# Performance work log

Hardware: AMD Instinct MI355X
Metric: run time of the kernel (lower is better)

The kernel has to match this reference:

```python
import jax, jax.numpy as jnp
import numpy as np
from jax import lax

B, L, D_MODEL = 2, 1024, 1024
EXPAND, D_STATE, D_CONV = 2, 16, 4
D_INNER = EXPAND * D_MODEL
DT_RANK = D_MODEL // 16  # ceil(1024/16) = 64
D_FF = 4 * D_MODEL


def setup_inputs() -> dict:
    key = jax.random.key(0)
    ks = jax.random.split(key, 20)
    s = lambda *sh: 1.0 / np.sqrt(sh[-1])
    inp = {
        "x": jax.random.normal(ks[0], (B, L, D_MODEL), jnp.float32),
        "ln1_w": jnp.ones((D_MODEL,), jnp.float32),
        "ln1_b": jnp.zeros((D_MODEL,), jnp.float32),
        "W_in": jax.random.normal(ks[1], (2 * D_INNER, D_MODEL), jnp.float32) * s(D_MODEL),
        "conv_w": jax.random.normal(ks[2], (D_INNER, D_CONV), jnp.float32) * s(D_CONV),
        "conv_b": jnp.zeros((D_INNER,), jnp.float32),
        "W_xproj": jax.random.normal(ks[3], (DT_RANK + 2 * D_STATE, D_INNER), jnp.float32) * s(D_INNER),
        "W_dt": jax.random.normal(ks[4], (D_INNER, DT_RANK), jnp.float32) * s(DT_RANK),
        "b_dt": jax.random.uniform(ks[5], (D_INNER,), jnp.float32, -4.0, -2.0),  # dt bias ~ small softplus
        "A_log": jnp.log(jnp.broadcast_to(jnp.arange(1, D_STATE + 1, dtype=jnp.float32), (D_INNER, D_STATE))),
        "D": jnp.ones((D_INNER,), jnp.float32),
        "W_out": jax.random.normal(ks[6], (D_MODEL, D_INNER), jnp.float32) * s(D_INNER),
        "ln2_w": jnp.ones((D_MODEL,), jnp.float32),
        "ln2_b": jnp.zeros((D_MODEL,), jnp.float32),
        "W1": jax.random.normal(ks[7], (D_FF, D_MODEL), jnp.float32) * s(D_MODEL),
        "b1": jnp.zeros((D_FF,), jnp.float32),
        "W2": jax.random.normal(ks[8], (D_MODEL, D_FF), jnp.float32) * s(D_FF),
        "b2": jnp.zeros((D_MODEL,), jnp.float32),
    }
    return inp


def _layernorm(x, w, b, eps=1e-5):
    mu = jnp.mean(x, axis=-1, keepdims=True)
    var = jnp.var(x, axis=-1, keepdims=True)
    return (x - mu) * lax.rsqrt(var + eps) * w + b


def _mamba(h, W_in, conv_w, conv_b, W_xproj, W_dt, b_dt, A_log, D, W_out):
    # in_proj -> [B, L, 2*d_inner]
    xz = jnp.einsum("bld,ed->ble", h, W_in)
    u, z = xz[..., :D_INNER], xz[..., D_INNER:]
    # causal depthwise conv over time
    uc = jnp.transpose(u, (0, 2, 1))  # [B, d_inner, L]
    uc = lax.conv_general_dilated(
        uc, conv_w[:, None, :], window_strides=(1,), padding=[(D_CONV - 1, 0)],
        dimension_numbers=("NCH", "OIH", "NCH"), feature_group_count=D_INNER)
    uc = jax.nn.silu(uc + conv_b[None, :, None])
    u = jnp.transpose(uc, (0, 2, 1))  # [B, L, d_inner]
    # input-dependent dt, B, C
    x_db = jnp.einsum("bld,ed->ble", u, W_xproj)
    dt = jax.nn.softplus(jnp.einsum("blr,dr->bld", x_db[..., :DT_RANK], W_dt) + b_dt)
    Bm = x_db[..., DT_RANK:DT_RANK + D_STATE]  # [B, L, d_state]
    Cm = x_db[..., DT_RANK + D_STATE:]         # [B, L, d_state]
    A = -jnp.exp(A_log)                        # [d_inner, d_state]

    def step(hst, t):
        dt_t, B_t, C_t, u_t = t  # [B,d_inner], [B,ds], [B,ds], [B,d_inner]
        dA = jnp.exp(dt_t[:, :, None] * A)                       # [B,d_inner,d_state]
        hst = dA * hst + dt_t[:, :, None] * B_t[:, None, :] * u_t[:, :, None]
        y_t = jnp.einsum("bds,bs->bd", hst, C_t)
        return hst, y_t

    h0 = jnp.zeros((u.shape[0], D_INNER, D_STATE), u.dtype)
    xs = (jnp.swapaxes(dt, 0, 1), jnp.swapaxes(Bm, 0, 1), jnp.swapaxes(Cm, 0, 1), jnp.swapaxes(u, 0, 1))
    _, ys = lax.scan(step, h0, xs)
    y = jnp.swapaxes(ys, 0, 1) + u * D  # skip term D*u
    y = y * jax.nn.silu(z)
    return jnp.einsum("ble,de->bld", y, W_out)


def reference(x, ln1_w, ln1_b, W_in, conv_w, conv_b, W_xproj, W_dt, b_dt, A_log, D,
              W_out, ln2_w, ln2_b, W1, b1, W2, b2):
    x = x + _mamba(_layernorm(x, ln1_w, ln1_b), W_in, conv_w, conv_b, W_xproj, W_dt, b_dt, A_log, D, W_out)
    h = _layernorm(x, ln2_w, ln2_b)
    ffn = jnp.einsum("blf,df->bld", jax.nn.relu(jnp.einsum("bld,fd->blf", h, W1) + b1), W2) + b2
    return x + ffn
```

## Files before the change

kernel.cpp:

```cpp
#include <hip/hip_runtime.h>

typedef unsigned short u16;
typedef unsigned int   u32;
typedef short   bf16x8 __attribute__((ext_vector_type(8)));
typedef float   f32x4  __attribute__((ext_vector_type(4)));
typedef u16     u16x4  __attribute__((ext_vector_type(4)));

__device__ __forceinline__ u16 f2b(float f) {
    u32 u = __builtin_bit_cast(u32, f);
    u32 r = u + 0x7FFFu + ((u >> 16) & 1u);
    return (u16)(r >> 16);
}
__device__ __forceinline__ float b2f(u16 h) {
    u32 u = ((u32)h) << 16;
    return __builtin_bit_cast(float, u);
}
__device__ __forceinline__ u16x4 f4_to_b4(float4 v) {
    u16x4 o; o.x = f2b(v.x); o.y = f2b(v.y); o.z = f2b(v.z); o.w = f2b(v.w);
    return o;
}

__device__ __forceinline__ float fexp2(float x) {
    float r;
    asm("v_exp_f32 %0, %1" : "=v"(r) : "v"(x));
    return r;
}
__device__ __forceinline__ float flog2(float x) {
    float r;
    asm("v_log_f32 %0, %1" : "=v"(r) : "v"(x));
    return r;
}

template <int CTRL>
__device__ __forceinline__ float dpp_add(float p) {
    int pi = __builtin_bit_cast(int, p);
    int q  = __builtin_amdgcn_update_dpp(pi, pi, CTRL, 0xF, 0xF, false);
    return p + __builtin_bit_cast(float, q);
}
#define DPP_XOR1 0xB1
#define DPP_XOR2 0x4E
#define DPP_HMIR 0x141
#define DPP_MIR  0x140

#define MROWS   2048
#define NSEG    16
#define SEGT    64
#define L2E     1.44269504088896340736f
#define LN2     0.69314718055994530942f

#define GLDS(g, l) __builtin_amdgcn_global_load_lds(                      \
    (const __attribute__((address_space(1))) void*)(g),                   \
    (__attribute__((address_space(3))) void*)(l), 16, 0, 0)

__global__ __launch_bounds__(256) void cvt_kernel(const float* __restrict__ in,
                                                  u16* __restrict__ out, int n4) {
    int i = blockIdx.x * 256 + threadIdx.x;
    if (i < n4) {
        float4 v = ((const float4*)in)[i];
        ((u16x4*)out)[i] = f4_to_b4(v);
    }
}

__global__ __launch_bounds__(256) void pad_xproj_kernel(const float* __restrict__ in,
                                                        u16* __restrict__ out) {
    int i = blockIdx.x * 256 + threadIdx.x;
    int r = i >> 9, c4 = i & 511;
    float4 v = make_float4(0.f, 0.f, 0.f, 0.f);
    if (r < 96) v = ((const float4*)(in + (size_t)r * 2048))[c4];
    ((u16x4*)(out + (size_t)r * 2048))[c4] = f4_to_b4(v);
}

__global__ __launch_bounds__(256) void ln_kernel(const float* __restrict__ x,
                                                 const float* __restrict__ w,
                                                 const float* __restrict__ b,
                                                 u16* __restrict__ out) {
    const int row = blockIdx.x;
    const int tid = threadIdx.x;
    const float4 v = ((const float4*)(x + (size_t)row * 1024))[tid];
    float s = v.x + v.y + v.z + v.w;
    float q = v.x * v.x + v.y * v.y + v.z * v.z + v.w * v.w;
#pragma unroll
    for (int off = 1; off < 64; off <<= 1) {
        s += __shfl_xor(s, off, 64);
        q += __shfl_xor(q, off, 64);
    }
    __shared__ float ss[4], qq[4];
    const int wave = tid >> 6;
    if ((tid & 63) == 0) { ss[wave] = s; qq[wave] = q; }
    __syncthreads();
    s = ss[0] + ss[1] + ss[2] + ss[3];
    q = qq[0] + qq[1] + qq[2] + qq[3];
    const float mean = s * (1.f / 1024.f);
    const float var  = q * (1.f / 1024.f) - mean * mean;
    const float rstd = rsqrtf(var + 1e-5f);
    const float4 wv = ((const float4*)w)[tid];
    const float4 bv = ((const float4*)b)[tid];
    float4 o;
    o.x = (v.x - mean) * rstd * wv.x + bv.x;
    o.y = (v.y - mean) * rstd * wv.y + bv.y;
    o.z = (v.z - mean) * rstd * wv.z + bv.z;
    o.w = (v.w - mean) * rstd * wv.w + bv.w;
    ((u16x4*)(out + (size_t)row * 1024))[tid] = f4_to_b4(o);
}

__global__ __launch_bounds__(256) void conv_kernel(const u16* __restrict__ xzu,
                                                   const float* __restrict__ cw,
                                                   const float* __restrict__ cb,
                                                   u16* __restrict__ up,
                                                   u16* __restrict__ utl) {
    const int idx = blockIdx.x * 256 + threadIdx.x;
    const int row = idx >> 9;
    const int d4  = idx & 511;
    const int d   = d4 * 4;
    const int bb  = row >> 10;
    const int t   = row & 1023;
    float w0[4], w1[4], w2[4], w3[4];
    *(float4*)w0 = ((const float4*)cw)[d + 0];
    *(float4*)w1 = ((const float4*)cw)[d + 1];
    *(float4*)w2 = ((const float4*)cw)[d + 2];
    *(float4*)w3 = ((const float4*)cw)[d + 3];
    float4 a = ((const float4*)cb)[d4];
#pragma unroll
    for (int j = 0; j < 4; ++j) {
        const int tt = t - 3 + j;
        if (tt >= 0) {
            const u16x4 uv = *(const u16x4*)(xzu + ((size_t)(bb * 1024 + tt)) * 2048 + d);
            a.x += b2f(uv.x) * w0[j];
            a.y += b2f(uv.y) * w1[j];
            a.z += b2f(uv.z) * w2[j];
            a.w += b2f(uv.w) * w3[j];
        }
    }
    float4 o;
    o.x = a.x / (1.f + __expf(-a.x));
    o.y = a.y / (1.f + __expf(-a.y));
    o.z = a.z / (1.f + __expf(-a.z));
    o.w = a.w / (1.f + __expf(-a.w));
    const u16x4 pk = f4_to_b4(o);
    ((u16x4*)up)[idx] = pk;
    *(u16x4*)(utl + (((size_t)(d >> 4)) * 2048 + row) * 16 + (d & 15)) = pk;
}

__global__ __launch_bounds__(256) void gemm_tb(const u16* __restrict__ A,
                                               const u16* __restrict__ Bw,
                                               float* __restrict__ Cptr,
                                               int M, int N, int K, int KS) {
    const int nbm = gridDim.x, nbn = gridDim.y;
    const int nwg = nbm * nbn;
    const int id  = blockIdx.x + nbm * blockIdx.y;
    const int sw  = (nwg >= 8) ? ((id & 7) * (nwg >> 3) + (id >> 3)) : id;
    const int bm  = sw % nbm, bn = sw / nbm;

    __shared__ u16 Asm[3][128 * 32];
    __shared__ u16 Bsm[3][128 * 32];
    const int tid  = threadIdx.x;
    const int kz   = blockIdx.z;
    const int lane = tid & 63;
    const int wave = tid >> 6;
    const int wm   = wave >> 1, wn = wave & 1;
    const u16* Ag = A  + (size_t)bm * 128 * K;
    const u16* Bg = Bw + (size_t)bn * 128 * K;
    const int r0 = tid >> 2;
    const int r1 = r0 + 64;
    const int sg = (tid & 3) * 8;
    const int k0 = kz * KS;
    const int nk = KS >> 5;
    const int fr = lane & 15, fk = (lane >> 4) * 8;

#define STG(bf, kk)                                                            \
    {                                                                          \
        const int kof = k0 + (kk) * 32;                                        \
        GLDS(Ag + (size_t)r0 * K + kof + sg, &Asm[bf][tid * 8]);               \
        GLDS(Ag + (size_t)r1 * K + kof + sg, &Asm[bf][(tid + 256) * 8]);       \
        GLDS(Bg + (size_t)r0 * K + kof + sg, &Bsm[bf][tid * 8]);               \
        GLDS(Bg + (size_t)r1 * K + kof + sg, &Bsm[bf][(tid + 256) * 8]);       \
    }

    f32x4 acc[4][4] = {};
    STG(0, 0); STG(1, 1); STG(2, 2);
    int buf = 0;
    for (int k = 0; k < nk; ++k) {
        if (k < nk - 2)       asm volatile("s_waitcnt vmcnt(8)" ::: "memory");
        else if (k == nk - 2) asm volatile("s_waitcnt vmcnt(4)" ::: "memory");
        else                  asm volatile("s_waitcnt vmcnt(0)" ::: "memory");
        __builtin_amdgcn_s_barrier();
        bf16x8 a[4], b[4];
#pragma unroll
        for (int m = 0; m < 4; ++m)
            a[m] = *(const bf16x8*)&Asm[buf][(wm * 64 + m * 16 + fr) * 32 + fk];
#pragma unroll
        for (int n = 0; n < 4; ++n)
            b[n] = *(const bf16x8*)&Bsm[buf][(wn * 64 + n * 16 + fr) * 32 + fk];
        asm volatile("s_waitcnt lgkmcnt(0)" ::: "memory");
        __builtin_amdgcn_s_barrier();
        if (k + 3 < nk) STG(buf, k + 3);
#pragma unroll
        for (int m = 0; m < 4; ++m)
#pragma unroll
            for (int n = 0; n < 4; ++n)
                acc[m][n] = __builtin_amdgcn_mfma_f32_16x16x32_bf16(a[m], b[n], acc[m][n], 0, 0, 0);
        buf = (buf == 2) ? 0 : buf + 1;
    }
#undef STG

    const int fq = lane >> 4;
#pragma unroll
    for (int m = 0; m < 4; ++m) {
#pragma unroll
        for (int n = 0; n < 4; ++n) {
            const int row0 = bm * 128 + wm * 64 + m * 16 + fq * 4;
            const int col  = bn * 128 + wn * 64 + n * 16 + fr;
#pragma unroll
            for (int j = 0; j < 4; ++j)
                Cptr[(size_t)kz * M * N + (size_t)(row0 + j) * N + col] = acc[m][n][j];
        }
    }
}

template <int EPI>
__global__ __launch_bounds__(256) void gemm_a64(const u16* __restrict__ A,
                                                const u16* __restrict__ Bw,
                                                void* __restrict__ Cptr,
                                                void* __restrict__ Cptr2,
                                                const float* __restrict__ bias,
                                                int M, int N, int K) {
    const int nbm = gridDim.x, nbn = gridDim.y;
    const int nwg = nbm * nbn;
    const int id  = blockIdx.x + nbm * blockIdx.y;
    const int sw  = (id & 7) * (nwg >> 3) + (id >> 3);
    const int bm  = sw % nbm, bn = sw / nbm;

    __shared__ u16 Asm[3][64 * 32];
    __shared__ u16 Bsm[3][128 * 32];
    const int tid  = threadIdx.x;
    const int lane = tid & 63;
    const int wave = tid >> 6;
    const int wm   = wave >> 1, wn = wave & 1;
    const u16* Ag = A  + (size_t)bm * 64 * K;
    const u16* Bg = Bw + (size_t)bn * 128 * K;
    const int r0 = tid >> 2;
    const int r1 = r0 + 64;
    const int sg = (tid & 3) * 8;
    const int nk = K >> 5;
    const int fr = lane & 15, fk = (lane >> 4) * 8;

#define STGA(bf, kk)                                                           \
    {                                                                          \
        const int kof = (kk) * 32;                                             \
        GLDS(Ag + (size_t)r0 * K + kof + sg, &Asm[bf][tid * 8]);               \
        GLDS(Bg + (size_t)r0 * K + kof + sg, &Bsm[bf][tid * 8]);               \
        GLDS(Bg + (size_t)r1 * K + kof + sg, &Bsm[bf][(tid + 256) * 8]);       \
    }

    f32x4 acc[2][4] = {};
    STGA(0, 0); STGA(1, 1); STGA(2, 2);
    int buf = 0;
    for (int k = 0; k < nk; ++k) {
        if (k < nk - 2)       asm volatile("s_waitcnt vmcnt(6)" ::: "memory");
        else if (k == nk - 2) asm volatile("s_waitcnt vmcnt(3)" ::: "memory");
        else                  asm volatile("s_waitcnt vmcnt(0)" ::: "memory");
        __builtin_amdgcn_s_barrier();
        bf16x8 a[2], b[4];
#pragma unroll
        for (int m = 0; m < 2; ++m)
            a[m] = *(const bf16x8*)&Asm[buf][(wm * 32 + m * 16 + fr) * 32 + fk];
#pragma unroll
        for (int n = 0; n < 4; ++n)
            b[n] = *(const bf16x8*)&Bsm[buf][(wn * 64 + n * 16 + fr) * 32 + fk];
        asm volatile("s_waitcnt lgkmcnt(0)" ::: "memory");
        __builtin_amdgcn_s_barrier();
        if (k + 3 < nk) STGA(buf, k + 3);
#pragma unroll
        for (int m = 0; m < 2; ++m)
#pragma unroll
            for (int n = 0; n < 4; ++n)
                acc[m][n] = __builtin_amdgcn_mfma_f32_16x16x32_bf16(a[m], b[n], acc[m][n], 0, 0, 0);
        buf = (buf == 2) ? 0 : buf + 1;
    }
#undef STGA

    const int fq = lane >> 4;
#pragma unroll
    for (int m = 0; m < 2; ++m) {
#pragma unroll
        for (int n = 0; n < 4; ++n) {
            const int row0 = bm * 64 + wm * 32 + m * 16 + fq * 4;
            const int col  = bn * 128 + wn * 64 + n * 16 + fr;
#pragma unroll
            for (int j = 0; j < 4; ++j) {
                float v = acc[m][n][j];
                if constexpr (EPI == 3) {
                    v += bias[col];
                    ((u16*)Cptr)[(size_t)(row0 + j) * N + col] = f2b(fmaxf(v, 0.f));
                } else {
                    if (col < 2048) {
                        ((u16*)Cptr)[(size_t)(row0 + j) * 2048 + col] = f2b(v);
                    } else {
                        const float sv = v / (1.f + __expf(-v));
                        const int zc = col - 2048;
                        ((u16*)Cptr2)[(((size_t)(zc >> 4)) * 2048 + row0 + j) * 16 + (zc & 15)]
                            = f2b(sv);
                    }
                }
            }
        }
    }
}

__global__ __launch_bounds__(256) void xproj_combine(const float* __restrict__ part,
                                                     u16* __restrict__ xdbr,
                                                     float* __restrict__ bcp) {
    int i = blockIdx.x * 256 + threadIdx.x;
    int row = i >> 5, c4 = i & 31;
    if (c4 >= 24) return;
    float4 s = make_float4(0.f, 0.f, 0.f, 0.f);
#pragma unroll
    for (int p = 0; p < 8; ++p) {
        float4 v = ((const float4*)(part + (size_t)p * MROWS * 128 + (size_t)row * 128))[c4];
        s.x += v.x; s.y += v.y; s.z += v.z; s.w += v.w;
    }
    if (c4 < 16) {
        ((u16x4*)(xdbr + (size_t)row * 64))[c4] = f4_to_b4(s);
    } else {
        const int e0 = (c4 - 16) * 4;
        float sv[4] = {s.x, s.y, s.z, s.w};
#pragma unroll
        for (int j = 0; j < 4; ++j) {
            const int e = e0 + j;
            const int st  = (e < 16) ? e : (e - 16);
            const int isc = (e < 16) ? 0 : 1;
            bcp[(size_t)(row >> 1) * 64 + st * 4 + (row & 1) * 2 + isc] = sv[j];
        }
    }
}

__device__ __forceinline__ void compute_dtu_tile(const u16* __restrict__ xdbr,
                                                 const u16* __restrict__ Wdtb,
                                                 const float* __restrict__ b_dt,
                                                 const u16* __restrict__ utile,
                                                 float* __restrict__ du_s,
                                                 size_t t0, int d0, int w, int l) {
    const int fr = l & 15, fk = (l >> 4) * 8;
    const bf16x8 a0 = *(const bf16x8*)(xdbr + (t0 + w * 16 + fr) * 64 + fk);
    const bf16x8 a1 = *(const bf16x8*)(xdbr + (t0 + w * 16 + fr) * 64 + 32 + fk);
    const bf16x8 b0 = *(const bf16x8*)(Wdtb + (size_t)(d0 + fr) * 64 + fk);
    const bf16x8 b1 = *(const bf16x8*)(Wdtb + (size_t)(d0 + fr) * 64 + 32 + fk);
    const float bdt = b_dt[d0 + fr];
    f32x4 acc = {};
    acc = __builtin_amdgcn_mfma_f32_16x16x32_bf16(a0, b0, acc, 0, 0, 0);
    acc = __builtin_amdgcn_mfma_f32_16x16x32_bf16(a1, b1, acc, 0, 0, 0);
#pragma unroll
    for (int j = 0; j < 4; ++j) {
        const int row = w * 16 + (l >> 4) * 4 + j;
        float v = acc[j] + bdt;
        const float sp = flog2(1.f + fexp2(v * L2E)) * LN2;
        v = (v > 20.f) ? v : sp;
        const float uval = b2f(utile[(t0 + row) * 16 + fr]);
        float2 dv; dv.x = v; dv.y = v * uval;
        *(float2*)&du_s[(row >> 1) * 66 + fr * 4 + (row & 1) * 2] = dv;
    }
}

__device__ __forceinline__ void stage_bc(const float* __restrict__ bcp,
                                         float* __restrict__ bc_s,
                                         size_t p0, int w, int l) {
    const int pr = (w << 3) + (l >> 4);
    const int pc = (l & 15) << 2;
    GLDS(bcp + (p0 + pr) * 64 + pc,     &bc_s[(w << 9)]);
    GLDS(bcp + (p0 + pr + 4) * 64 + pc, &bc_s[(w << 9) + 256]);
}

__global__ __launch_bounds__(256) void scan_pass1(const u16* __restrict__ xdbr,
                                                  const u16* __restrict__ Wdtb,
                                                  const float* __restrict__ b_dt,
                                                  const u16* __restrict__ utl,
                                                  const float* __restrict__ bcp,
                                                  const float* __restrict__ A_log,
                                                  float* __restrict__ Qarr,
                                                  float* __restrict__ Sarr) {
    __shared__ __align__(16) float du_s[32 * 66];
    __shared__ __align__(16) float bc_s[32 * 64];

    const int tid = threadIdx.x;
    const int l   = tid & 63;
    const int w   = tid >> 6;
    const int s   = l & 15;
    const int g   = (w << 2) | (l >> 4);
    const int d0  = blockIdx.x << 4;
    const int b   = blockIdx.y;
    const int seg = blockIdx.z;
    const int d   = d0 + g;
    const size_t t0 = (size_t)b * 1024 + (size_t)seg * SEGT;
    const u16* utile = utl + (size_t)(d0 >> 4) * 2048 * 16;

    stage_bc(bcp, bc_s, t0 >> 1, w, l);
    compute_dtu_tile(xdbr, Wdtb, b_dt, utile, du_s, t0, d0, w, l);

    const float As2 = -__expf(A_log[d * 16 + s]) * L2E;
    asm volatile("s_waitcnt vmcnt(0) lgkmcnt(0)" ::: "memory");
    __builtin_amdgcn_s_barrier();

    float Q = 0.f, S = 0.f;
#pragma unroll 8
    for (int t2 = 0; t2 < 32; ++t2) {
        const float4 du4 = *(const float4*)&du_s[t2 * 66 + g * 4];
        const float4 BC2 = *(const float4*)&bc_s[t2 * 64 + s * 4];
        S += du4.x;
        Q = fexp2(du4.x * As2) * Q + du4.y * BC2.x;
        S += du4.z;
        Q = fexp2(du4.z * As2) * Q + du4.w * BC2.z;
    }
    Qarr[(((size_t)seg * 2 + b) * 2048 + d) * 16 + s] = Q;
    if (s == 0) Sarr[((size_t)seg * 2 + b) * 2048 + d] = S;
}

__global__ __launch_bounds__(256) void scan_prefix(const float* __restrict__ Qarr,
                                                   const float* __restrict__ Sarr,
                                                   const float* __restrict__ A_log,
                                                   float* __restrict__ H0) {
    const int tid = threadIdx.x;
    const int d   = (blockIdx.x << 4) + (tid >> 4);
    const int s   = tid & 15;
    const int b   = blockIdx.y;
    const float As2 = -__expf(A_log[d * 16 + s]) * L2E;
    float h = 0.f;
#pragma unroll
    for (int i = 0; i < NSEG; ++i) {
        const size_t base = ((size_t)i * 2 + b) * 2048 + d;
        H0[base * 16 + s] = h;
        h = fexp2(As2 * Sarr[base]) * h + Qarr[base * 16 + s];
    }
}

__global__ __launch_bounds__(256) void scan_pass2(const u16* __restrict__ xdbr,
                                                  const u16* __restrict__ Wdtb,
                                                  const float* __restrict__ b_dt,
                                                  const u16* __restrict__ utl,
                                                  const float* __restrict__ bcp,
                                                  const u16* __restrict__ zst,
                                                  const float* __restrict__ A_log,
                                                  const float* __restrict__ Dp,
                                                  const float* __restrict__ H0,
                                                  u16* __restrict__ ymul) {
    __shared__ __align__(16) float du_s[32 * 66];
    __shared__ __align__(16) float bc_s[32 * 64];
    __shared__ __align__(16) u16   u_s[1024];
    __shared__ __align__(16) u16   z_s[1024];

    const int tid = threadIdx.x;
    const int l   = tid & 63;
    const int w   = tid >> 6;
    const int s   = l & 15;
    const int g   = (w << 2) | (l >> 4);
    const int d0  = blockIdx.x << 4;
    const int b   = blockIdx.y;
    const int seg = blockIdx.z;
    const int d   = d0 + g;
    const size_t t0 = (size_t)b * 1024 + (size_t)seg * SEGT;
    const u16* utile = utl + (size_t)(d0 >> 4) * 2048 * 16;
    const u16* ztile = zst + (size_t)(d0 >> 4) * 2048 * 16;

    stage_bc(bcp, bc_s, t0 >> 1, w, l);
    if (w < 2)
        GLDS(utile + t0 * 16 + ((w & 1) * 64 + l) * 8, &u_s[(w & 1) << 9]);
    else
        GLDS(ztile + t0 * 16 + ((w & 1) * 64 + l) * 8, &z_s[(w & 1) << 9]);

    compute_dtu_tile(xdbr, Wdtb, b_dt, utile, du_s, t0, d0, w, l);

    const float As2 = -__expf(A_log[d * 16 + s]) * L2E;
    float h = H0[(((size_t)seg * 2 + b) * 2048 + d) * 16 + s];

    asm volatile("s_waitcnt vmcnt(0) lgkmcnt(0)" ::: "memory");
    __builtin_amdgcn_s_barrier();

    float pk[4];
#pragma unroll
    for (int c = 0; c < 4; ++c) {
        pk[c] = 0.f;
#pragma unroll
        for (int q = 0; q < 8; ++q) {
            const int t2 = c * 8 + q;
            const float4 du4 = *(const float4*)&du_s[t2 * 66 + g * 4];
            const float4 BC2 = *(const float4*)&bc_s[t2 * 64 + s * 4];
            h = fexp2(du4.x * As2) * h + du4.y * BC2.x;
            float p = h * BC2.y;
            p = dpp_add<DPP_XOR1>(p);
            p = dpp_add<DPP_XOR2>(p);
            p = dpp_add<DPP_HMIR>(p);
            p = dpp_add<DPP_MIR>(p);
            {
                const unsigned long long km = 0x0001000100010001ULL << (2 * q);
                asm("v_cndmask_b32 %0, %0, %1, %2" : "+v"(pk[c]) : "v"(p), "s"(km));
            }
            h = fexp2(du4.z * As2) * h + du4.w * BC2.z;
            p = h * BC2.w;
            p = dpp_add<DPP_XOR1>(p);
            p = dpp_add<DPP_XOR2>(p);
            p = dpp_add<DPP_HMIR>(p);
            p = dpp_add<DPP_MIR>(p);
            {
                const unsigned long long km = 0x0001000100010001ULL << (2 * q + 1);
                asm("v_cndmask_b32 %0, %0, %1, %2" : "+v"(pk[c]) : "v"(p), "s"(km));
            }
        }
    }

    __builtin_amdgcn_s_barrier();
    float* p_s = du_s;
#pragma unroll
    for (int c = 0; c < 4; ++c) {
        const int row = c * 16 + s;
        p_s[row * 16 + (g ^ (row & 12))] = pk[c];
    }

    asm volatile("s_waitcnt lgkmcnt(0)" ::: "memory");
    __builtin_amdgcn_s_barrier();

    {
        const int tt = tid >> 2, cc = (tid & 3) << 2;
        const float4 pv = *(const float4*)&p_s[tt * 16 + (cc ^ (tt & 12))];
        const u16x4  uv = *(const u16x4*)&u_s[tt * 16 + cc];
        const u16x4  zs = *(const u16x4*)&z_s[tt * 16 + cc];
        const float4 Dv = *(const float4*)(Dp + d0 + cc);
        float4 o;
        o.x = (pv.x + b2f(uv.x) * Dv.x) * b2f(zs.x);
        o.y = (pv.y + b2f(uv.y) * Dv.y) * b2f(zs.y);
        o.z = (pv.z + b2f(uv.z) * Dv.z) * b2f(zs.z);
        o.w = (pv.w + b2f(uv.w) * Dv.w) * b2f(zs.w);
        *(u16x4*)(ymul + (t0 + tt) * 2048 + d0 + cc) = f4_to_b4(o);
    }
}

__global__ __launch_bounds__(256) void ffn2_combine(const float* __restrict__ part,
                                                    const float* __restrict__ x2,
                                                    const float* __restrict__ b2,
                                                    float* __restrict__ out) {
    int i = blockIdx.x * 256 + threadIdx.x;
    float4 s = ((const float4*)x2)[i];
    float4 bv = ((const float4*)b2)[i & 255];
    s.x += bv.x; s.y += bv.y; s.z += bv.z; s.w += bv.w;
#pragma unroll
    for (int p = 0; p < 4; ++p) {
        float4 v = ((const float4*)(part + (size_t)p * MROWS * 1024))[i];
        s.x += v.x; s.y += v.y; s.z += v.z; s.w += v.w;
    }
    ((float4*)out)[i] = s;
}

__global__ __launch_bounds__(256) void outproj_combine_ln2(const float* __restrict__ x,
                                                           const float* __restrict__ part,
                                                           const float* __restrict__ w,
                                                           const float* __restrict__ b,
                                                           float* __restrict__ x2,
                                                           u16* __restrict__ h2) {
    const int row = blockIdx.x;
    const int tid = threadIdx.x;
    float4 v = ((const float4*)(x + (size_t)row * 1024))[tid];
    float4 p0 = ((const float4*)(part + (size_t)row * 1024))[tid];
    float4 p1 = ((const float4*)(part + (size_t)MROWS * 1024 + (size_t)row * 1024))[tid];
    v.x += p0.x + p1.x; v.y += p0.y + p1.y; v.z += p0.z + p1.z; v.w += p0.w + p1.w;
    ((float4*)(x2 + (size_t)row * 1024))[tid] = v;
    float s = v.x + v.y + v.z + v.w;
    float q = v.x * v.x + v.y * v.y + v.z * v.z + v.w * v.w;
#pragma unroll
    for (int off = 1; off < 64; off <<= 1) {
        s += __shfl_xor(s, off, 64);
        q += __shfl_xor(q, off, 64);
    }
    __shared__ float ss[4], qq[4];
    const int wave = tid >> 6;
    if ((tid & 63) == 0) { ss[wave] = s; qq[wave] = q; }
    __syncthreads();
    s = ss[0] + ss[1] + ss[2] + ss[3];
    q = qq[0] + qq[1] + qq[2] + qq[3];
    const float mean = s * (1.f / 1024.f);
    const float var  = q * (1.f / 1024.f) - mean * mean;
    const float rstd = rsqrtf(var + 1e-5f);
    const float4 wv = ((const float4*)w)[tid];
    const float4 bv = ((const float4*)b)[tid];
    float4 o;
    o.x = (v.x - mean) * rstd * wv.x + bv.x;
    o.y = (v.y - mean) * rstd * wv.y + bv.y;
    o.z = (v.z - mean) * rstd * wv.z + bv.z;
    o.w = (v.w - mean) * rstd * wv.w + bv.w;
    ((u16x4*)(h2 + (size_t)row * 1024))[tid] = f4_to_b4(o);
}

extern "C" void kernel_launch(void* const* d_in, const int* in_sizes, int n_in,
                              void* d_out, int out_size, void* d_ws, size_t ws_size,
                              hipStream_t stream) {
    const float* x      = (const float*)d_in[0];
    const float* ln1_w  = (const float*)d_in[1];
    const float* ln1_b  = (const float*)d_in[2];
    const float* W_in   = (const float*)d_in[3];
    const float* conv_w = (const float*)d_in[4];
    const float* conv_b = (const float*)d_in[5];
    const float* W_xproj= (const float*)d_in[6];
    const float* W_dt   = (const float*)d_in[7];
    const float* b_dt   = (const float*)d_in[8];
    const float* A_log  = (const float*)d_in[9];
    const float* Dvec   = (const float*)d_in[10];
    const float* W_out  = (const float*)d_in[11];
    const float* ln2_w  = (const float*)d_in[12];
    const float* ln2_b  = (const float*)d_in[13];
    const float* W1     = (const float*)d_in[14];
    const float* b1     = (const float*)d_in[15];
    const float* W2     = (const float*)d_in[16];
    const float* b2     = (const float*)d_in[17];
    float* out = (float*)d_out;
    char*  ws  = (char*)d_ws;
    const size_t MB = 1024ull * 1024ull;

    u16*   h1b   = (u16*)(ws + 0);
    u16*   xzu   = (u16*)(ws + 4 * MB);
    u16*   zst   = (u16*)(ws + 12 * MB);
    u16*   upb   = (u16*)(ws + 20 * MB);
    u16*   utl   = (u16*)(ws + 28 * MB);
    float* parts = (float*)(ws + 36 * MB);
    float* bcp   = (float*)(ws + 44 * MB);
    u16*   xdbr  = (u16*)(ws + 44 * MB + 256 * 1024);
    u16*   Wdtb  = (u16*)(ws + 44 * MB + 512 * 1024);
    u16*   ymul  = (u16*)(ws + 45 * MB);
    float* Qarr  = (float*)(ws + 53 * MB);
    float* Sarr  = (float*)(ws + 57 * MB);
    float* H0    = (float*)(ws + 58 * MB);
    float* x2    = (float*)(ws + 62 * MB);
    u16*   Winb  = (u16*)(ws + 70 * MB);
    u16*   Woutb = (u16*)(ws + 78 * MB);
    u16*   W1b   = (u16*)(ws + 82 * MB);
    u16*   W2b   = (u16*)(ws + 90 * MB);
    u16*   Wxpb  = (u16*)(ws + 98 * MB);
    u16*   h2b   = h1b;
    float* opart = (float*)(ws + 4 * MB);
    u16*   f1    = (u16*)(ws + 4 * MB);
    float* fpart = (float*)(ws + 20 * MB);

    cvt_kernel<<<4096, 256, 0, stream>>>(W_in,  Winb,  4096 * 1024 / 4);
    cvt_kernel<<<2048, 256, 0, stream>>>(W_out, Woutb, 1024 * 2048 / 4);
    cvt_kernel<<<4096, 256, 0, stream>>>(W1,    W1b,   4096 * 1024 / 4);
    cvt_kernel<<<4096, 256, 0, stream>>>(W2,    W2b,   1024 * 4096 / 4);
    cvt_kernel<<<128,  256, 0, stream>>>(W_dt,  Wdtb,  2048 * 64 / 4);
    pad_xproj_kernel<<<256, 256, 0, stream>>>(W_xproj, Wxpb);

    ln_kernel<<<2048, 256, 0, stream>>>(x, ln1_w, ln1_b, h1b);
    gemm_a64<5><<<dim3(32, 32), 256, 0, stream>>>(h1b, Winb, xzu, zst, nullptr,
                                                  MROWS, 4096, 1024);
    conv_kernel<<<4096, 256, 0, stream>>>(xzu, conv_w, conv_b, upb, utl);
    gemm_tb<<<dim3(16, 1, 8), 256, 0, stream>>>(upb, Wxpb, parts, MROWS, 128, 2048, 256);
    xproj_combine<<<256, 256, 0, stream>>>(parts, xdbr, bcp);
    scan_pass1<<<dim3(128, 2, NSEG), 256, 0, stream>>>(xdbr, Wdtb, b_dt, utl, bcp, A_log,
                                                       Qarr, Sarr);
    scan_prefix<<<dim3(128, 2), 256, 0, stream>>>(Qarr, Sarr, A_log, H0);
    scan_pass2<<<dim3(128, 2, NSEG), 256, 0, stream>>>(xdbr, Wdtb, b_dt, utl, bcp, zst,
                                                       A_log, Dvec, H0, ymul);
    gemm_tb<<<dim3(16, 8, 2), 256, 0, stream>>>(ymul, Woutb, opart, MROWS, 1024, 2048, 1024);
    outproj_combine_ln2<<<2048, 256, 0, stream>>>(x, opart, ln2_w, ln2_b, x2, h2b);
    gemm_a64<3><<<dim3(32, 32), 256, 0, stream>>>(h2b, W1b, f1, nullptr, b1,
                                                  MROWS, 4096, 1024);
    gemm_tb<<<dim3(16, 8, 4), 256, 0, stream>>>(f1, W2b, fpart, MROWS, 1024, 4096, 1024);
    ffn2_combine<<<2048, 256, 0, stream>>>(fpart, x2, b2, out);
}
```

Baseline: 242.9 us.

## Unify GEMMs on 128x128 tiles, read x-proj from tiled conv output, merge weight casts

```diff
diff --git a/kernel.cpp b/kernel.cpp
--- a/kernel.cpp
+++ b/kernel.cpp
@@ -52,13 +52,25 @@
     (const __attribute__((address_space(1))) void*)(g),                   \
     (__attribute__((address_space(3))) void*)(l), 16, 0, 0)
 
-__global__ __launch_bounds__(256) void cvt_kernel(const float* __restrict__ in,
-                                                  u16* __restrict__ out, int n4) {
-    int i = blockIdx.x * 256 + threadIdx.x;
-    if (i < n4) {
-        float4 v = ((const float4*)in)[i];
-        ((u16x4*)out)[i] = f4_to_b4(v);
-    }
+__global__ __launch_bounds__(256) void cvt_all(const float* __restrict__ W_in,
+                                               const float* __restrict__ W_out,
+                                               const float* __restrict__ W1,
+                                               const float* __restrict__ W2,
+                                               const float* __restrict__ W_dt,
+                                               u16* __restrict__ Winb,
+                                               u16* __restrict__ Woutb,
+                                               u16* __restrict__ W1b,
+                                               u16* __restrict__ W2b,
+                                               u16* __restrict__ Wdtb) {
+    const int i = blockIdx.x * 256 + threadIdx.x;
+    const float* src; u16* dst; int off;
+    if (i < 1048576)      { src = W_in;  dst = Winb;  off = i; }
+    else if (i < 1572864) { src = W_out; dst = Woutb; off = i - 1048576; }
+    else if (i < 2621440) { src = W1;    dst = W1b;   off = i - 1572864; }
+    else if (i < 3670016) { src = W2;    dst = W2b;   off = i - 2621440; }
+    else                  { src = W_dt;  dst = Wdtb;  off = i - 3670016; }
+    float4 v = ((const float4*)src)[off];
+    ((u16x4*)dst)[off] = f4_to_b4(v);
 }
 
 __global__ __launch_bounds__(256) void pad_xproj_kernel(const float* __restrict__ in,
@@ -106,7 +118,6 @@
 __global__ __launch_bounds__(256) void conv_kernel(const u16* __restrict__ xzu,
                                                    const float* __restrict__ cw,
                                                    const float* __restrict__ cb,
-                                                   u16* __restrict__ up,
                                                    u16* __restrict__ utl) {
     const int idx = blockIdx.x * 256 + threadIdx.x;
     const int row = idx >> 9;
@@ -136,14 +147,15 @@
     o.y = a.y / (1.f + __expf(-a.y));
     o.z = a.z / (1.f + __expf(-a.z));
     o.w = a.w / (1.f + __expf(-a.w));
-    const u16x4 pk = f4_to_b4(o);
-    ((u16x4*)up)[idx] = pk;
-    *(u16x4*)(utl + (((size_t)(d >> 4)) * 2048 + row) * 16 + (d & 15)) = pk;
-}
-
+    *(u16x4*)(utl + (((size_t)(d >> 4)) * 2048 + row) * 16 + (d & 15)) = f4_to_b4(o);
+}
+
+template <int EPI>
 __global__ __launch_bounds__(256) void gemm_tb(const u16* __restrict__ A,
                                                const u16* __restrict__ Bw,
-                                               float* __restrict__ Cptr,
+                                               void* __restrict__ Cptr,
+                                               void* __restrict__ Cptr2,
+                                               const float* __restrict__ bias,
                                                int M, int N, int K, int KS) {
     const int nbm = gridDim.x, nbn = gridDim.y;
     const int nwg = nbm * nbn;
@@ -211,88 +223,12 @@
             const int row0 = bm * 128 + wm * 64 + m * 16 + fq * 4;
             const int col  = bn * 128 + wn * 64 + n * 16 + fr;
 #pragma unroll
-            for (int j = 0; j < 4; ++j)
-                Cptr[(size_t)kz * M * N + (size_t)(row0 + j) * N + col] = acc[m][n][j];
-        }
-    }
-}
-
-template <int EPI>
-__global__ __launch_bounds__(256) void gemm_a64(const u16* __restrict__ A,
-                                                const u16* __restrict__ Bw,
-                                                void* __restrict__ Cptr,
-                                                void* __restrict__ Cptr2,
-                                                const float* __restrict__ bias,
-                                                int M, int N, int K) {
-    const int nbm = gridDim.x, nbn = gridDim.y;
-    const int nwg = nbm * nbn;
-    const int id  = blockIdx.x + nbm * blockIdx.y;
-    const int sw  = (id & 7) * (nwg >> 3) + (id >> 3);
-    const int bm  = sw % nbm, bn = sw / nbm;
-
-    __shared__ u16 Asm[3][64 * 32];
-    __shared__ u16 Bsm[3][128 * 32];
-    const int tid  = threadIdx.x;
-    const int lane = tid & 63;
-    const int wave = tid >> 6;
-    const int wm   = wave >> 1, wn = wave & 1;
-    const u16* Ag = A  + (size_t)bm * 64 * K;
-    const u16* Bg = Bw + (size_t)bn * 128 * K;
-    const int r0 = tid >> 2;
-    const int r1 = r0 + 64;
-    const int sg = (tid & 3) * 8;
-    const int nk = K >> 5;
-    const int fr = lane & 15, fk = (lane >> 4) * 8;
-
-#define STGA(bf, kk)                                                           \
-    {                                                                          \
-        const int kof = (kk) * 32;                                             \
-        GLDS(Ag + (size_t)r0 * K + kof + sg, &Asm[bf][tid * 8]);               \
-        GLDS(Bg + (size_t)r0 * K + kof + sg, &Bsm[bf][tid * 8]);               \
-        GLDS(Bg + (size_t)r1 * K + kof + sg, &Bsm[bf][(tid + 256) * 8]);       \
-    }
-
-    f32x4 acc[2][4] = {};
-    STGA(0, 0); STGA(1, 1); STGA(2, 2);
-    int buf = 0;
-    for (int k = 0; k < nk; ++k) {
-        if (k < nk - 2)       asm volatile("s_waitcnt vmcnt(6)" ::: "memory");
-        else if (k == nk - 2) asm volatile("s_waitcnt vmcnt(3)" ::: "memory");
-        else                  asm volatile("s_waitcnt vmcnt(0)" ::: "memory");
-        __builtin_amdgcn_s_barrier();
-        bf16x8 a[2], b[4];
-#pragma unroll
-        for (int m = 0; m < 2; ++m)
-            a[m] = *(const bf16x8*)&Asm[buf][(wm * 32 + m * 16 + fr) * 32 + fk];
-#pragma unroll
-        for (int n = 0; n < 4; ++n)
-            b[n] = *(const bf16x8*)&Bsm[buf][(wn * 64 + n * 16 + fr) * 32 + fk];
-        asm volatile("s_waitcnt lgkmcnt(0)" ::: "memory");
-        __builtin_amdgcn_s_barrier();
-        if (k + 3 < nk) STGA(buf, k + 3);
-#pragma unroll
-        for (int m = 0; m < 2; ++m)
-#pragma unroll
-            for (int n = 0; n < 4; ++n)
-                acc[m][n] = __builtin_amdgcn_mfma_f32_16x16x32_bf16(a[m], b[n], acc[m][n], 0, 0, 0);
-        buf = (buf == 2) ? 0 : buf + 1;
-    }
-#undef STGA
-
-    const int fq = lane >> 4;
-#pragma unroll
-    for (int m = 0; m < 2; ++m) {
-#pragma unroll
-        for (int n = 0; n < 4; ++n) {
-            const int row0 = bm * 64 + wm * 32 + m * 16 + fq * 4;
-            const int col  = bn * 128 + wn * 64 + n * 16 + fr;
-#pragma unroll
             for (int j = 0; j < 4; ++j) {
                 float v = acc[m][n][j];
                 if constexpr (EPI == 3) {
                     v += bias[col];
                     ((u16*)Cptr)[(size_t)(row0 + j) * N + col] = f2b(fmaxf(v, 0.f));
-                } else {
+                } else if constexpr (EPI == 5) {
                     if (col < 2048) {
                         ((u16*)Cptr)[(size_t)(row0 + j) * 2048 + col] = f2b(v);
                     } else {
@@ -301,8 +237,86 @@
                         ((u16*)Cptr2)[(((size_t)(zc >> 4)) * 2048 + row0 + j) * 16 + (zc & 15)]
                             = f2b(sv);
                     }
+                } else {
+                    ((float*)Cptr)[(size_t)kz * M * N + (size_t)(row0 + j) * N + col] = v;
                 }
             }
+        }
+    }
+}
+
+__global__ __launch_bounds__(256) void gemm_xp(const u16* __restrict__ utl,
+                                               const u16* __restrict__ Bw,
+                                               float* __restrict__ part) {
+    const int nwg = 16;
+    const int id  = blockIdx.x;
+    const int sw  = (id & 7) * (nwg >> 3) + (id >> 3);
+    const int bm  = sw;
+    __shared__ u16 Asm[3][128 * 32];
+    __shared__ u16 Bsm[3][128 * 32];
+    const int tid  = threadIdx.x;
+    const int kz   = blockIdx.z;
+    const int lane = tid & 63;
+    const int wave = tid >> 6;
+    const int wm   = wave >> 1, wn = wave & 1;
+    const u16* Bg = Bw;
+    const int r0 = tid >> 2;
+    const int pc = tid & 3;
+    const int sg = pc * 8;
+    const int k0 = kz * 256;
+    const int fr = lane & 15, fk = (lane >> 4) * 8;
+
+#define STGX(bf, kk)                                                                     \
+    {                                                                                    \
+        const int kof = k0 + (kk) * 32;                                                  \
+        const int kc  = kof >> 4;                                                        \
+        GLDS(utl + ((size_t)(kc + (pc >> 1)) * 2048 + bm * 128 + r0) * 16 + (pc & 1) * 8,\
+             &Asm[bf][tid * 8]);                                                         \
+        GLDS(utl + ((size_t)(kc + (pc >> 1)) * 2048 + bm * 128 + r0 + 64) * 16 + (pc & 1) * 8,\
+             &Asm[bf][(tid + 256) * 8]);                                                 \
+        GLDS(Bg + (size_t)r0 * 2048 + kof + sg, &Bsm[bf][tid * 8]);                      \
+        GLDS(Bg + (size_t)(r0 + 64) * 2048 + kof + sg, &Bsm[bf][(tid + 256) * 8]);       \
+    }
+
+    f32x4 acc[4][4] = {};
+    STGX(0, 0); STGX(1, 1); STGX(2, 2);
+    int buf = 0;
+    const int nk = 8;
+    for (int k = 0; k < nk; ++k) {
+        if (k < nk - 2)       asm volatile("s_waitcnt vmcnt(8)" ::: "memory");
+        else if (k == nk - 2) asm volatile("s_waitcnt vmcnt(4)" ::: "memory");
+        else                  asm volatile("s_waitcnt vmcnt(0)" ::: "memory");
+        __builtin_amdgcn_s_barrier();
+        bf16x8 a[4], b[4];
+#pragma unroll
+        for (int m = 0; m < 4; ++m)
+            a[m] = *(const bf16x8*)&Asm[buf][(wm * 64 + m * 16 + fr) * 32 + fk];
+#pragma unroll
+        for (int n = 0; n < 4; ++n)
+            b[n] = *(const bf16x8*)&Bsm[buf][(wn * 64 + n * 16 + fr) * 32 + fk];
+        asm volatile("s_waitcnt lgkmcnt(0)" ::: "memory");
+        __builtin_amdgcn_s_barrier();
+        if (k + 3 < nk) STGX(buf, k + 3);
+#pragma unroll
+        for (int m = 0; m < 4; ++m)
+#pragma unroll
+            for (int n = 0; n < 4; ++n)
+                acc[m][n] = __builtin_amdgcn_mfma_f32_16x16x32_bf16(a[m], b[n], acc[m][n], 0, 0, 0);
+        buf = (buf == 2) ? 0 : buf + 1;
+    }
+#undef STGX
+
+    const int fq = lane >> 4;
+    float* Cp = part + (size_t)kz * MROWS * 128;
+#pragma unroll
+    for (int m = 0; m < 4; ++m) {
+#pragma unroll
+        for (int n = 0; n < 4; ++n) {
+            const int row0 = bm * 128 + wm * 64 + m * 16 + fq * 4;
+            const int col  = wn * 64 + n * 16 + fr;
+#pragma unroll
+            for (int j = 0; j < 4; ++j)
+                Cp[(size_t)(row0 + j) * 128 + col] = acc[m][n][j];
         }
     }
 }
@@ -615,49 +629,47 @@
     u16*   h1b   = (u16*)(ws + 0);
     u16*   xzu   = (u16*)(ws + 4 * MB);
     u16*   zst   = (u16*)(ws + 12 * MB);
-    u16*   upb   = (u16*)(ws + 20 * MB);
-    u16*   utl   = (u16*)(ws + 28 * MB);
-    float* parts = (float*)(ws + 36 * MB);
-    float* bcp   = (float*)(ws + 44 * MB);
-    u16*   xdbr  = (u16*)(ws + 44 * MB + 256 * 1024);
-    u16*   Wdtb  = (u16*)(ws + 44 * MB + 512 * 1024);
-    u16*   ymul  = (u16*)(ws + 45 * MB);
-    float* Qarr  = (float*)(ws + 53 * MB);
-    float* Sarr  = (float*)(ws + 57 * MB);
-    float* H0    = (float*)(ws + 58 * MB);
-    float* x2    = (float*)(ws + 62 * MB);
-    u16*   Winb  = (u16*)(ws + 70 * MB);
-    u16*   Woutb = (u16*)(ws + 78 * MB);
-    u16*   W1b   = (u16*)(ws + 82 * MB);
-    u16*   W2b   = (u16*)(ws + 90 * MB);
-    u16*   Wxpb  = (u16*)(ws + 98 * MB);
+    u16*   utl   = (u16*)(ws + 20 * MB);
+    float* parts = (float*)(ws + 28 * MB);
+    float* bcp   = (float*)(ws + 36 * MB);
+    u16*   xdbr  = (u16*)(ws + 36 * MB + 256 * 1024);
+    u16*   Wdtb  = (u16*)(ws + 36 * MB + 512 * 1024);
+    u16*   ymul  = (u16*)(ws + 37 * MB);
+    float* Qarr  = (float*)(ws + 45 * MB);
+    float* Sarr  = (float*)(ws + 49 * MB);
+    float* H0    = (float*)(ws + 50 * MB);
+    float* x2    = (float*)(ws + 54 * MB);
+    u16*   Winb  = (u16*)(ws + 62 * MB);
+    u16*   Woutb = (u16*)(ws + 70 * MB);
+    u16*   W1b   = (u16*)(ws + 74 * MB);
+    u16*   W2b   = (u16*)(ws + 82 * MB);
+    u16*   Wxpb  = (u16*)(ws + 90 * MB);
     u16*   h2b   = h1b;
     float* opart = (float*)(ws + 4 * MB);
     u16*   f1    = (u16*)(ws + 4 * MB);
     float* fpart = (float*)(ws + 20 * MB);
 
-    cvt_kernel<<<4096, 256, 0, stream>>>(W_in,  Winb,  4096 * 1024 / 4);
-    cvt_kernel<<<2048, 256, 0, stream>>>(W_out, Woutb, 1024 * 2048 / 4);
-    cvt_kernel<<<4096, 256, 0, stream>>>(W1,    W1b,   4096 * 1024 / 4);
-    cvt_kernel<<<4096, 256, 0, stream>>>(W2,    W2b,   1024 * 4096 / 4);
-    cvt_kernel<<<128,  256, 0, stream>>>(W_dt,  Wdtb,  2048 * 64 / 4);
+    cvt_all<<<14464, 256, 0, stream>>>(W_in, W_out, W1, W2, W_dt,
+                                       Winb, Woutb, W1b, W2b, Wdtb);
     pad_xproj_kernel<<<256, 256, 0, stream>>>(W_xproj, Wxpb);
 
     ln_kernel<<<2048, 256, 0, stream>>>(x, ln1_w, ln1_b, h1b);
-    gemm_a64<5><<<dim3(32, 32), 256, 0, stream>>>(h1b, Winb, xzu, zst, nullptr,
-                                                  MROWS, 4096, 1024);
-    conv_kernel<<<4096, 256, 0, stream>>>(xzu, conv_w, conv_b, upb, utl);
-    gemm_tb<<<dim3(16, 1, 8), 256, 0, stream>>>(upb, Wxpb, parts, MROWS, 128, 2048, 256);
+    gemm_tb<5><<<dim3(16, 32, 1), 256, 0, stream>>>(h1b, Winb, xzu, zst, nullptr,
+                                                    MROWS, 4096, 1024, 1024);
+    conv_kernel<<<4096, 256, 0, stream>>>(xzu, conv_w, conv_b, utl);
+    gemm_xp<<<dim3(16, 1, 8), 256, 0, stream>>>(utl, Wxpb, parts);
     xproj_combine<<<256, 256, 0, stream>>>(parts, xdbr, bcp);
     scan_pass1<<<dim3(128, 2, NSEG), 256, 0, stream>>>(xdbr, Wdtb, b_dt, utl, bcp, A_log,
                                                        Qarr, Sarr);
     scan_prefix<<<dim3(128, 2), 256, 0, stream>>>(Qarr, Sarr, A_log, H0);
     scan_pass2<<<dim3(128, 2, NSEG), 256, 0, stream>>>(xdbr, Wdtb, b_dt, utl, bcp, zst,
                                                        A_log, Dvec, H0, ymul);
-    gemm_tb<<<dim3(16, 8, 2), 256, 0, stream>>>(ymul, Woutb, opart, MROWS, 1024, 2048, 1024);
+    gemm_tb<10><<<dim3(16, 8, 2), 256, 0, stream>>>(ymul, Woutb, opart, nullptr, nullptr,
+                                                    MROWS, 1024, 2048, 1024);
     outproj_combine_ln2<<<2048, 256, 0, stream>>>(x, opart, ln2_w, ln2_b, x2, h2b);
-    gemm_a64<3><<<dim3(32, 32), 256, 0, stream>>>(h2b, W1b, f1, nullptr, b1,
-                                                  MROWS, 4096, 1024);
-    gemm_tb<<<dim3(16, 8, 4), 256, 0, stream>>>(f1, W2b, fpart, MROWS, 1024, 4096, 1024);
+    gemm_tb<3><<<dim3(16, 32, 1), 256, 0, stream>>>(h2b, W1b, f1, nullptr, b1,
+                                                    MROWS, 4096, 1024, 1024);
+    gemm_tb<10><<<dim3(16, 8, 4), 256, 0, stream>>>(f1, W2b, fpart, nullptr, nullptr,
+                                                    MROWS, 1024, 4096, 1024);
     ffn2_combine<<<2048, 256, 0, stream>>>(fpart, x2, b2, out);
 }
```

Result: faster. 226.2 us (-6.9%).
